# Kernel optimization log

Hardware: AMD Instinct MI355X
Metric: run time of the kernel (lower is better)

Reference implementation:

```python
import jax, jax.numpy as jnp
import numpy as np

HEADS = 16
DIM_HEAD = 64
QUERY_DIM = 1024


def setup_inputs() -> dict:
    key = jax.random.key(0)
    ks = jax.random.split(key, 5)
    B, S, D = 4, 2048, QUERY_DIM
    inner = HEADS * DIM_HEAD
    s = 0.02
    return {
        "x": jax.random.normal(ks[0], (B, S, D), dtype=jnp.float32),
        "Wq": jax.random.normal(ks[1], (D, inner), dtype=jnp.float32) * s,
        "Wk": jax.random.normal(ks[2], (D, inner), dtype=jnp.float32) * s,
        "Wv": jax.random.normal(ks[3], (D, inner), dtype=jnp.float32) * s,
        "Wo": jax.random.normal(ks[4], (inner, D), dtype=jnp.float32) * s,
    }


def reference(x, Wq, Wk, Wv, Wo):
    B, S, D = x.shape
    h, d = HEADS, DIM_HEAD
    scale = d ** (-0.5)
    # projections -> [B, h, S, d]
    q = (x @ Wq).reshape(B, S, h, d).transpose(0, 2, 1, 3)
    k = (x @ Wk).reshape(B, S, h, d).transpose(0, 2, 1, 3)
    v = (x @ Wv).reshape(B, S, h, d).transpose(0, 2, 1, 3)
    # scores [B, h, S, S]
    attn = jnp.einsum("bhqd,bhkd->bhqk", q, k) * scale
    attn = jax.nn.softmax(attn, axis=-1)
    out = jnp.einsum("bhqk,bhkd->bhqd", attn, v)
    out = out.transpose(0, 2, 1, 3).reshape(B, S, h * d)
    return out @ Wo
```

## Files before the change

### kernel.cpp

```cpp
#include <hip/hip_runtime.h>
#include <cstddef>

#define BATCH  4
#define SLEN   2048
#define NHEADS 16
#define DHEAD  64
#define DMODEL 1024

typedef __attribute__((ext_vector_type(8))) short short8;
typedef __attribute__((ext_vector_type(4))) float f32x4;

__device__ inline unsigned short f2bf(float f) {
    union { float f; unsigned int u; } v; v.f = f;
    unsigned int r = v.u + 0x7fffu + ((v.u >> 16) & 1u);
    return (unsigned short)(r >> 16);
}

__device__ inline float fast_exp2(float x) {
#if __has_builtin(__builtin_amdgcn_exp2f)
    return __builtin_amdgcn_exp2f(x);
#else
    return __expf(x * 0.69314718f);
#endif
}

__device__ inline void gload_lds16(const unsigned short* g, unsigned short* l) {
    __builtin_amdgcn_global_load_lds(
        (const __attribute__((address_space(1))) void*)g,
        (__attribute__((address_space(3))) void*)l, 16, 0, 0);
}

__global__ __launch_bounds__(256)
void convert_bf16(const float* __restrict__ src, unsigned short* __restrict__ dst, int n8)
{
    const int i = blockIdx.x * 256 + threadIdx.x;
    if (i >= n8) return;
    const float4 a = ((const float4*)src)[2 * i];
    const float4 b = ((const float4*)src)[2 * i + 1];
    short8 o;
    o[0] = (short)f2bf(a.x); o[1] = (short)f2bf(a.y);
    o[2] = (short)f2bf(a.z); o[3] = (short)f2bf(a.w);
    o[4] = (short)f2bf(b.x); o[5] = (short)f2bf(b.y);
    o[6] = (short)f2bf(b.z); o[7] = (short)f2bf(b.w);
    ((short8*)dst)[i] = o;
}

__global__ __launch_bounds__(256)
void wtrans(const float* __restrict__ W0, const float* __restrict__ W1,
            const float* __restrict__ W2, const float* __restrict__ W3,
            unsigned short* __restrict__ T0, unsigned short* __restrict__ T1,
            unsigned short* __restrict__ T2, unsigned short* __restrict__ T3)
{
    const int z = blockIdx.z;
    const float* W = (z == 0) ? W0 : (z == 1) ? W1 : (z == 2) ? W2 : W3;
    unsigned short* Wt = (z == 0) ? T0 : (z == 1) ? T1 : (z == 2) ? T2 : T3;

    __shared__ unsigned short T[64 * 72];
    const int tid = threadIdx.x;
    const int n0 = blockIdx.x * 64, k0 = blockIdx.y * 64;

    #pragma unroll
    for (int it = 0; it < 2; it++) {
        const int t2 = it * 256 + tid;
        const int row = t2 >> 3, col8 = (t2 & 7) * 8;
        const float4 a = *(const float4*)(W + (size_t)(k0 + row) * DMODEL + n0 + col8);
        const float4 b = *(const float4*)(W + (size_t)(k0 + row) * DMODEL + n0 + col8 + 4);
        short8 o;
        o[0] = (short)f2bf(a.x); o[1] = (short)f2bf(a.y);
        o[2] = (short)f2bf(a.z); o[3] = (short)f2bf(a.w);
        o[4] = (short)f2bf(b.x); o[5] = (short)f2bf(b.y);
        o[6] = (short)f2bf(b.z); o[7] = (short)f2bf(b.w);
        *(short8*)&T[row * 72 + col8] = o;
    }
    __syncthreads();
    #pragma unroll
    for (int it = 0; it < 2; it++) {
        const int t2 = it * 256 + tid;
        const int nn = t2 >> 3, k8 = (t2 & 7) * 8;
        short8 v;
        #pragma unroll
        for (int j = 0; j < 8; j++) v[j] = (short)T[(k8 + j) * 72 + nn];
        *(short8*)(Wt + (size_t)(n0 + nn) * DMODEL + k0 + k8) = v;
    }
}

__global__ __launch_bounds__(256)
void transpose_v(const unsigned short* __restrict__ vb, unsigned short* __restrict__ vtb)
{
    __shared__ unsigned short T[64 * 72];
    const int tid = threadIdx.x, st = blockIdx.x, bh = blockIdx.y;
    const int b = bh >> 4, h = bh & 15;
    const size_t bh_base = ((size_t)b * SLEN * NHEADS + h) * 64;

    #pragma unroll
    for (int it = 0; it < 2; it++) {
        const int t2 = it * 256 + tid;
        const int row = t2 >> 3, col8 = (t2 & 7) * 8;
        *(short8*)&T[row * 72 + col8] =
            *(const short8*)(vb + bh_base + (size_t)(st * 64 + row) * (NHEADS * 64) + col8);
    }
    __syncthreads();
    #pragma unroll
    for (int it = 0; it < 2; it++) {
        const int t2 = it * 256 + tid;
        const int dd = t2 >> 3, s8 = (t2 & 7) * 8;
        short8 v;
        #pragma unroll
        for (int j = 0; j < 8; j++) v[j] = (short)T[(s8 + j) * 72 + dd];
        *(short8*)(vtb + ((size_t)bh * 64 + dd) * SLEN + st * 64 + s8) = v;
    }
}

template<int OUTF32>
__global__ __launch_bounds__(256)
void gemm_bf16(const unsigned short* __restrict__ A,
               const unsigned short* __restrict__ B0,
               const unsigned short* __restrict__ B1,
               const unsigned short* __restrict__ B2,
               void* __restrict__ C0v, void* __restrict__ C1v, void* __restrict__ C2v)
{
    constexpr int N = DMODEL, K = DMODEL;
    __shared__ unsigned short As[128 * 64];
    __shared__ unsigned short Bs[128 * 64];

    const int z = blockIdx.z;
    const unsigned short* Bw = (z == 0) ? B0 : (z == 1) ? B1 : B2;
    void* Cv = (z == 0) ? C0v : (z == 1) ? C1v : C2v;

    const int tid  = threadIdx.x;
    const int lane = tid & 63;
    const int wave = tid >> 6;
    const int c  = lane & 15, qd = lane >> 4;
    const int wr = wave >> 1, wc = wave & 1;
    const int m0 = blockIdx.y * 128, n0 = blockIdx.x * 128;

    const unsigned short* ag[4];
    const unsigned short* bg[4];
    unsigned short* al[4];
    unsigned short* bl[4];
    #pragma unroll
    for (int j = 0; j < 4; j++) {
        const int cid = j * 256 + tid;
        const int row = cid >> 3;
        const int k8  = (cid & 7) ^ (row & 7);
        ag[j] = A  + (size_t)(m0 + row) * K + k8 * 8;
        bg[j] = Bw + (size_t)(n0 + row) * K + k8 * 8;
        al[j] = &As[cid * 8];
        bl[j] = &Bs[cid * 8];
    }

    f32x4 acc[4][4];
    #pragma unroll
    for (int mb = 0; mb < 4; mb++)
        #pragma unroll
        for (int nb = 0; nb < 4; nb++)
            #pragma unroll
            for (int r = 0; r < 4; r++) acc[mb][nb][r] = 0.f;

    for (int k0 = 0; k0 < K; k0 += 64) {
        __syncthreads();
        #pragma unroll
        for (int j = 0; j < 4; j++) {
            gload_lds16(ag[j], al[j]);
            gload_lds16(bg[j], bl[j]);
            ag[j] += 64; bg[j] += 64;
        }
        __syncthreads();

        #pragma unroll
        for (int ks = 0; ks < 2; ks++) {
            const int sw = (ks * 4 + qd) ^ (c & 7);
            short8 af[4], bf[4];
            #pragma unroll
            for (int mb = 0; mb < 4; mb++)
                af[mb] = *(const short8*)&As[((wr * 64 + mb * 16 + c) * 8 + sw) * 8];
            #pragma unroll
            for (int nb = 0; nb < 4; nb++)
                bf[nb] = *(const short8*)&Bs[((wc * 64 + nb * 16 + c) * 8 + sw) * 8];
            #pragma unroll
            for (int mb = 0; mb < 4; mb++)
                #pragma unroll
                for (int nb = 0; nb < 4; nb++)
                    acc[mb][nb] = __builtin_amdgcn_mfma_f32_16x16x32_bf16(
                        af[mb], bf[nb], acc[mb][nb], 0, 0, 0);
        }
    }

    const int mbase = m0 + wr * 64 + qd * 4;
    const int nbase = n0 + wc * 64 + c;
    if (OUTF32) {
        float* C = (float*)Cv;
        #pragma unroll
        for (int mb = 0; mb < 4; mb++)
            #pragma unroll
            for (int nb = 0; nb < 4; nb++)
                #pragma unroll
                for (int r = 0; r < 4; r++)
                    C[(size_t)(mbase + mb * 16 + r) * N + nbase + nb * 16] = acc[mb][nb][r];
    } else {
        unsigned short* C = (unsigned short*)Cv;
        #pragma unroll
        for (int mb = 0; mb < 4; mb++)
            #pragma unroll
            for (int nb = 0; nb < 4; nb++)
                #pragma unroll
                for (int r = 0; r < 4; r++)
                    C[(size_t)(mbase + mb * 16 + r) * N + nbase + nb * 16] = f2bf(acc[mb][nb][r]);
    }
}

__global__ __launch_bounds__(256)
void attn_mfma2(const unsigned short* __restrict__ qb,
                const unsigned short* __restrict__ kb,
                const unsigned short* __restrict__ vtb,
                unsigned short* __restrict__ O)
{
    __shared__ unsigned short lds[17408];
    unsigned short* Ks = lds;
    unsigned short* Vs = lds + 4096;

    const int tid = threadIdx.x;
    const int w   = tid >> 6, ln = tid & 63;
    const int c   = ln & 15, qd = ln >> 4;
    unsigned short* Pw = lds + 8192 + w * 2048;

    const int qt = blockIdx.x, bh = blockIdx.y;
    const int b = bh >> 4, h = bh & 15;
    const size_t bh_base = ((size_t)b * SLEN * NHEADS + h) * 64;
    constexpr int RS = NHEADS * 64;
    constexpr float SCL2 = 0.18033688f;

    const int srow = ln >> 3;
    const int sk8  = (ln & 7) ^ srow;
    const unsigned short* kg0 = kb + bh_base + (size_t)(w * 8 + srow) * RS + sk8 * 8;
    const unsigned short* kg1 = kg0 + (size_t)32 * RS;
    const unsigned short* vg0 = vtb + ((size_t)bh * 64 + w * 8 + srow) * SLEN + sk8 * 8;
    const unsigned short* vg1 = vg0 + (size_t)32 * SLEN;
    unsigned short* kl0 = &Ks[(w * 64 + ln) * 8];
    unsigned short* kl1 = kl0 + 2048;
    unsigned short* vl0 = &Vs[(w * 64 + ln) * 8];
    unsigned short* vl1 = vl0 + 2048;

    short8 qf[2][2];
    #pragma unroll
    for (int qh = 0; qh < 2; qh++)
        #pragma unroll
        for (int ks = 0; ks < 2; ks++)
            qf[qh][ks] = *(const short8*)(qb + bh_base +
                (size_t)(qt * 128 + w * 32 + qh * 16 + c) * RS + ks * 32 + qd * 8);

    f32x4 acc[4][2];
    #pragma unroll
    for (int mb = 0; mb < 4; mb++)
        #pragma unroll
        for (int qh = 0; qh < 2; qh++)
            #pragma unroll
            for (int r = 0; r < 4; r++) acc[mb][qh][r] = 0.f;
    float lsum[2] = {0.f, 0.f};
    const int X0 = (0 * 4 + qd) ^ (c & 7);
    const int X1 = (1 * 4 + qd) ^ (c & 7);

    for (int kt = 0; kt < SLEN / 64; kt++) {
        __syncthreads();
        gload_lds16(kg0, kl0); gload_lds16(kg1, kl1);
        gload_lds16(vg0, vl0); gload_lds16(vg1, vl1);
        kg0 += (size_t)64 * RS; kg1 += (size_t)64 * RS; vg0 += 64; vg1 += 64;
        __syncthreads();

        f32x4 sacc[4][2];
        #pragma unroll
        for (int kbI = 0; kbI < 4; kbI++)
            #pragma unroll
            for (int qh = 0; qh < 2; qh++)
                #pragma unroll
                for (int r = 0; r < 4; r++) sacc[kbI][qh][r] = 0.f;
        #pragma unroll
        for (int ks = 0; ks < 2; ks++) {
            const int X = ks ? X1 : X0;
            #pragma unroll
            for (int kbI = 0; kbI < 4; kbI++) {
                short8 kf = *(const short8*)&Ks[((kbI * 16 + c) * 8 + X) * 8];
                sacc[kbI][0] = __builtin_amdgcn_mfma_f32_16x16x32_bf16(kf, qf[0][ks], sacc[kbI][0], 0, 0, 0);
                sacc[kbI][1] = __builtin_amdgcn_mfma_f32_16x16x32_bf16(kf, qf[1][ks], sacc[kbI][1], 0, 0, 0);
            }
        }

        #pragma unroll
        for (int kbI = 0; kbI < 4; kbI++)
            #pragma unroll
            for (int qh = 0; qh < 2; qh++) {
                const float p0 = fast_exp2(sacc[kbI][qh][0] * SCL2);
                const float p1 = fast_exp2(sacc[kbI][qh][1] * SCL2);
                const float p2 = fast_exp2(sacc[kbI][qh][2] * SCL2);
                const float p3 = fast_exp2(sacc[kbI][qh][3] * SCL2);
                lsum[qh] += (p0 + p1) + (p2 + p3);
                uint2 pk;
                pk.x = __builtin_amdgcn_perm(__float_as_uint(p1), __float_as_uint(p0), 0x07060302u);
                pk.y = __builtin_amdgcn_perm(__float_as_uint(p3), __float_as_uint(p2), 0x07060302u);
                *(uint2*)&Pw[(qh * 16 + c) * 64 +
                             ((kbI * 2 + (qd >> 1)) ^ (c & 7)) * 8 + (qd & 1) * 4] = pk;
            }
        __builtin_amdgcn_wave_barrier();

        #pragma unroll
        for (int ks = 0; ks < 2; ks++) {
            const int X = ks ? X1 : X0;
            short8 pf0 = *(const short8*)&Pw[(0 * 16 + c) * 64 + X * 8];
            short8 pf1 = *(const short8*)&Pw[(1 * 16 + c) * 64 + X * 8];
            #pragma unroll
            for (int mb = 0; mb < 4; mb++) {
                short8 vf = *(const short8*)&Vs[((mb * 16 + c) * 8 + X) * 8];
                acc[mb][0] = __builtin_amdgcn_mfma_f32_16x16x32_bf16(vf, pf0, acc[mb][0], 0, 0, 0);
                acc[mb][1] = __builtin_amdgcn_mfma_f32_16x16x32_bf16(vf, pf1, acc[mb][1], 0, 0, 0);
            }
        }
    }

    __syncthreads();
    float inv[2];
    #pragma unroll
    for (int qh = 0; qh < 2; qh++) {
        float l = lsum[qh];
        l += __shfl_xor(l, 16);
        l += __shfl_xor(l, 32);
        inv[qh] = 1.001953125f / l;
    }
    float* Ot = (float*)lds;
    #pragma unroll
    for (int mb = 0; mb < 4; mb++)
        #pragma unroll
        for (int qh = 0; qh < 2; qh++)
            #pragma unroll
            for (int r = 0; r < 4; r++)
                Ot[(w * 32 + qh * 16 + c) * 68 + mb * 16 + qd * 4 + r] = acc[mb][qh][r] * inv[qh];
    __syncthreads();
    #pragma unroll
    for (int it = 0; it < 4; it++) {
        const int t2 = it * 256 + tid;
        const int row = t2 >> 3, col8 = (t2 & 7) * 8;
        short8 o;
        #pragma unroll
        for (int j = 0; j < 8; j++) o[j] = (short)f2bf(Ot[row * 68 + col8 + j]);
        *(short8*)(O + bh_base + (size_t)(qt * 128 + row) * RS + col8) = o;
    }
}

extern "C" void kernel_launch(void* const* d_in, const int* in_sizes, int n_in,
                              void* d_out, int out_size, void* d_ws, size_t ws_size,
                              hipStream_t stream)
{
    const float* x  = (const float*)d_in[0];
    const float* Wq = (const float*)d_in[1];
    const float* Wk = (const float*)d_in[2];
    const float* Wv = (const float*)d_in[3];
    const float* Wo = (const float*)d_in[4];
    float* out = (float*)d_out;

    const size_t per = (size_t)BATCH * SLEN * NHEADS * DHEAD;
    const size_t wsz = (size_t)DMODEL * DMODEL;
    unsigned short* qb  = (unsigned short*)d_ws;
    unsigned short* kb  = qb  + per;
    unsigned short* vb  = kb  + per;
    unsigned short* vtb = vb  + per;
    unsigned short* xb  = vtb + per;
    unsigned short* wtq = xb  + per;
    unsigned short* wtk = wtq + wsz;
    unsigned short* wtv = wtk + wsz;
    unsigned short* wto = wtv + wsz;

    dim3 blk(256);
    convert_bf16<<<dim3((int)(per / 2048)), blk, 0, stream>>>(x, xb, (int)(per / 8));
    wtrans<<<dim3(16, 16, 4), blk, 0, stream>>>(Wq, Wk, Wv, Wo, wtq, wtk, wtv, wto);

    gemm_bf16<0><<<dim3(8, 64, 3), blk, 0, stream>>>(xb, wtq, wtk, wtv, qb, kb, vb);

    transpose_v<<<dim3(32, 64), blk, 0, stream>>>(vb, vtb);
    attn_mfma2<<<dim3(SLEN / 128, BATCH * NHEADS), blk, 0, stream>>>(qb, kb, vtb, qb);

    gemm_bf16<1><<<dim3(8, 64, 1), blk, 0, stream>>>(qb, wto, wto, wto, out, out, out);
}
```

Before: 315.9 us.

## Fuse V transpose into QKV GEMM epilogue and double attention query tile

The QKV projection GEMM now writes V directly in transposed [b,h,d,s] layout from its epilogue, so the separate transpose_v kernel and its intermediate buffer go away. The attention kernel grows to 256 queries per block (64 per wave), which reuses each loaded K/V tile across twice as many queries and halves the number of K/V loads per query. Its epilogue converts to bf16 in per-wave LDS and stores without block-wide syncs. In exchange there is more register and LDS pressure, fewer blocks (512), and the V epilogue stores are narrower and strided.

```diff
diff --git a/kernel.cpp b/kernel.cpp
--- a/kernel.cpp
+++ b/kernel.cpp
@@ -84,34 +84,7 @@
     }
 }
 
-__global__ __launch_bounds__(256)
-void transpose_v(const unsigned short* __restrict__ vb, unsigned short* __restrict__ vtb)
-{
-    __shared__ unsigned short T[64 * 72];
-    const int tid = threadIdx.x, st = blockIdx.x, bh = blockIdx.y;
-    const int b = bh >> 4, h = bh & 15;
-    const size_t bh_base = ((size_t)b * SLEN * NHEADS + h) * 64;
-
-    #pragma unroll
-    for (int it = 0; it < 2; it++) {
-        const int t2 = it * 256 + tid;
-        const int row = t2 >> 3, col8 = (t2 & 7) * 8;
-        *(short8*)&T[row * 72 + col8] =
-            *(const short8*)(vb + bh_base + (size_t)(st * 64 + row) * (NHEADS * 64) + col8);
-    }
-    __syncthreads();
-    #pragma unroll
-    for (int it = 0; it < 2; it++) {
-        const int t2 = it * 256 + tid;
-        const int dd = t2 >> 3, s8 = (t2 & 7) * 8;
-        short8 v;
-        #pragma unroll
-        for (int j = 0; j < 8; j++) v[j] = (short)T[(s8 + j) * 72 + dd];
-        *(short8*)(vtb + ((size_t)bh * 64 + dd) * SLEN + st * 64 + s8) = v;
-    }
-}
-
-template<int OUTF32>
+template<int KIND>
 __global__ __launch_bounds__(256)
 void gemm_bf16(const unsigned short* __restrict__ A,
                const unsigned short* __restrict__ B0,
@@ -188,7 +161,7 @@
 
     const int mbase = m0 + wr * 64 + qd * 4;
     const int nbase = n0 + wc * 64 + c;
-    if (OUTF32) {
+    if (KIND == 1) {
         float* C = (float*)Cv;
         #pragma unroll
         for (int mb = 0; mb < 4; mb++)
@@ -197,32 +170,47 @@
                 #pragma unroll
                 for (int r = 0; r < 4; r++)
                     C[(size_t)(mbase + mb * 16 + r) * N + nbase + nb * 16] = acc[mb][nb][r];
+    } else if (z != 2) {
+        unsigned short* C = (unsigned short*)Cv;
+        #pragma unroll
+        for (int mb = 0; mb < 4; mb++)
+            #pragma unroll
+            for (int nb = 0; nb < 4; nb++)
+                #pragma unroll
+                for (int r = 0; r < 4; r++)
+                    C[(size_t)(mbase + mb * 16 + r) * N + nbase + nb * 16] = f2bf(acc[mb][nb][r]);
     } else {
         unsigned short* C = (unsigned short*)Cv;
-        #pragma unroll
-        for (int mb = 0; mb < 4; mb++)
-            #pragma unroll
-            for (int nb = 0; nb < 4; nb++)
-                #pragma unroll
-                for (int r = 0; r < 4; r++)
-                    C[(size_t)(mbase + mb * 16 + r) * N + nbase + nb * 16] = f2bf(acc[mb][nb][r]);
-    }
-}
-
-__global__ __launch_bounds__(256)
-void attn_mfma2(const unsigned short* __restrict__ qb,
+        const int b = mbase >> 11;
+        #pragma unroll
+        for (int mb = 0; mb < 4; mb++) {
+            const int s = (mbase + mb * 16) & 2047;
+            #pragma unroll
+            for (int nb = 0; nb < 4; nb++) {
+                const int n = nbase + nb * 16;
+                const int h = n >> 6, dd = n & 63;
+                ushort4 val = make_ushort4(f2bf(acc[mb][nb][0]), f2bf(acc[mb][nb][1]),
+                                           f2bf(acc[mb][nb][2]), f2bf(acc[mb][nb][3]));
+                *(ushort4*)(C + ((size_t)((b * 16 + h) * 64 + dd)) * SLEN + s) = val;
+            }
+        }
+    }
+}
+
+__global__ __launch_bounds__(256, 2)
+void attn_mfma3(const unsigned short* __restrict__ qb,
                 const unsigned short* __restrict__ kb,
                 const unsigned short* __restrict__ vtb,
                 unsigned short* __restrict__ O)
 {
-    __shared__ unsigned short lds[17408];
+    __shared__ unsigned short lds[26624];
     unsigned short* Ks = lds;
     unsigned short* Vs = lds + 4096;
 
     const int tid = threadIdx.x;
     const int w   = tid >> 6, ln = tid & 63;
     const int c   = ln & 15, qd = ln >> 4;
-    unsigned short* Pw = lds + 8192 + w * 2048;
+    unsigned short* Pw = lds + 8192 + w * 4608;
 
     const int qt = blockIdx.x, bh = blockIdx.y;
     const int b = bh >> 4, h = bh & 15;
@@ -241,24 +229,24 @@
     unsigned short* vl0 = &Vs[(w * 64 + ln) * 8];
     unsigned short* vl1 = vl0 + 2048;
 
-    short8 qf[2][2];
-    #pragma unroll
-    for (int qh = 0; qh < 2; qh++)
+    short8 qf[4][2];
+    #pragma unroll
+    for (int qh = 0; qh < 4; qh++)
         #pragma unroll
         for (int ks = 0; ks < 2; ks++)
             qf[qh][ks] = *(const short8*)(qb + bh_base +
-                (size_t)(qt * 128 + w * 32 + qh * 16 + c) * RS + ks * 32 + qd * 8);
-
-    f32x4 acc[4][2];
+                (size_t)(qt * 256 + w * 64 + qh * 16 + c) * RS + ks * 32 + qd * 8);
+
+    f32x4 acc[4][4];
     #pragma unroll
     for (int mb = 0; mb < 4; mb++)
         #pragma unroll
-        for (int qh = 0; qh < 2; qh++)
+        for (int qh = 0; qh < 4; qh++)
             #pragma unroll
             for (int r = 0; r < 4; r++) acc[mb][qh][r] = 0.f;
-    float lsum[2] = {0.f, 0.f};
-    const int X0 = (0 * 4 + qd) ^ (c & 7);
-    const int X1 = (1 * 4 + qd) ^ (c & 7);
+    float lsum[4] = {0.f, 0.f, 0.f, 0.f};
+    const int X0 = qd ^ (c & 7);
+    const int X1 = (4 + qd) ^ (c & 7);
 
     for (int kt = 0; kt < SLEN / 64; kt++) {
         __syncthreads();
@@ -267,81 +255,80 @@
         kg0 += (size_t)64 * RS; kg1 += (size_t)64 * RS; vg0 += 64; vg1 += 64;
         __syncthreads();
 
-        f32x4 sacc[4][2];
-        #pragma unroll
-        for (int kbI = 0; kbI < 4; kbI++)
-            #pragma unroll
-            for (int qh = 0; qh < 2; qh++)
-                #pragma unroll
-                for (int r = 0; r < 4; r++) sacc[kbI][qh][r] = 0.f;
-        #pragma unroll
-        for (int ks = 0; ks < 2; ks++) {
-            const int X = ks ? X1 : X0;
-            #pragma unroll
-            for (int kbI = 0; kbI < 4; kbI++) {
+        #pragma unroll
+        for (int kbI = 0; kbI < 4; kbI++) {
+            f32x4 sacc[4];
+            #pragma unroll
+            for (int qh = 0; qh < 4; qh++)
+                #pragma unroll
+                for (int r = 0; r < 4; r++) sacc[qh][r] = 0.f;
+            #pragma unroll
+            for (int ks = 0; ks < 2; ks++) {
+                const int X = ks ? X1 : X0;
                 short8 kf = *(const short8*)&Ks[((kbI * 16 + c) * 8 + X) * 8];
-                sacc[kbI][0] = __builtin_amdgcn_mfma_f32_16x16x32_bf16(kf, qf[0][ks], sacc[kbI][0], 0, 0, 0);
-                sacc[kbI][1] = __builtin_amdgcn_mfma_f32_16x16x32_bf16(kf, qf[1][ks], sacc[kbI][1], 0, 0, 0);
+                #pragma unroll
+                for (int qh = 0; qh < 4; qh++)
+                    sacc[qh] = __builtin_amdgcn_mfma_f32_16x16x32_bf16(
+                        kf, qf[qh][ks], sacc[qh], 0, 0, 0);
             }
-        }
-
-        #pragma unroll
-        for (int kbI = 0; kbI < 4; kbI++)
-            #pragma unroll
-            for (int qh = 0; qh < 2; qh++) {
-                const float p0 = fast_exp2(sacc[kbI][qh][0] * SCL2);
-                const float p1 = fast_exp2(sacc[kbI][qh][1] * SCL2);
-                const float p2 = fast_exp2(sacc[kbI][qh][2] * SCL2);
-                const float p3 = fast_exp2(sacc[kbI][qh][3] * SCL2);
+            const int pchunk = ((kbI * 2 + (qd >> 1)) ^ (c & 7)) * 8 + (qd & 1) * 4;
+            #pragma unroll
+            for (int qh = 0; qh < 4; qh++) {
+                const float p0 = fast_exp2(sacc[qh][0] * SCL2);
+                const float p1 = fast_exp2(sacc[qh][1] * SCL2);
+                const float p2 = fast_exp2(sacc[qh][2] * SCL2);
+                const float p3 = fast_exp2(sacc[qh][3] * SCL2);
                 lsum[qh] += (p0 + p1) + (p2 + p3);
                 uint2 pk;
                 pk.x = __builtin_amdgcn_perm(__float_as_uint(p1), __float_as_uint(p0), 0x07060302u);
                 pk.y = __builtin_amdgcn_perm(__float_as_uint(p3), __float_as_uint(p2), 0x07060302u);
-                *(uint2*)&Pw[(qh * 16 + c) * 64 +
-                             ((kbI * 2 + (qd >> 1)) ^ (c & 7)) * 8 + (qd & 1) * 4] = pk;
+                *(uint2*)&Pw[(qh * 16 + c) * 64 + pchunk] = pk;
             }
+        }
         __builtin_amdgcn_wave_barrier();
 
         #pragma unroll
         for (int ks = 0; ks < 2; ks++) {
             const int X = ks ? X1 : X0;
-            short8 pf0 = *(const short8*)&Pw[(0 * 16 + c) * 64 + X * 8];
-            short8 pf1 = *(const short8*)&Pw[(1 * 16 + c) * 64 + X * 8];
+            short8 pf[4];
+            #pragma unroll
+            for (int qh = 0; qh < 4; qh++)
+                pf[qh] = *(const short8*)&Pw[(qh * 16 + c) * 64 + X * 8];
             #pragma unroll
             for (int mb = 0; mb < 4; mb++) {
                 short8 vf = *(const short8*)&Vs[((mb * 16 + c) * 8 + X) * 8];
-                acc[mb][0] = __builtin_amdgcn_mfma_f32_16x16x32_bf16(vf, pf0, acc[mb][0], 0, 0, 0);
-                acc[mb][1] = __builtin_amdgcn_mfma_f32_16x16x32_bf16(vf, pf1, acc[mb][1], 0, 0, 0);
+                #pragma unroll
+                for (int qh = 0; qh < 4; qh++)
+                    acc[mb][qh] = __builtin_amdgcn_mfma_f32_16x16x32_bf16(
+                        vf, pf[qh], acc[mb][qh], 0, 0, 0);
             }
         }
     }
 
-    __syncthreads();
-    float inv[2];
-    #pragma unroll
-    for (int qh = 0; qh < 2; qh++) {
+    float inv[4];
+    #pragma unroll
+    for (int qh = 0; qh < 4; qh++) {
         float l = lsum[qh];
         l += __shfl_xor(l, 16);
         l += __shfl_xor(l, 32);
         inv[qh] = 1.001953125f / l;
     }
-    float* Ot = (float*)lds;
+    __builtin_amdgcn_wave_barrier();
     #pragma unroll
     for (int mb = 0; mb < 4; mb++)
         #pragma unroll
-        for (int qh = 0; qh < 2; qh++)
+        for (int qh = 0; qh < 4; qh++)
             #pragma unroll
             for (int r = 0; r < 4; r++)
-                Ot[(w * 32 + qh * 16 + c) * 68 + mb * 16 + qd * 4 + r] = acc[mb][qh][r] * inv[qh];
-    __syncthreads();
-    #pragma unroll
-    for (int it = 0; it < 4; it++) {
-        const int t2 = it * 256 + tid;
+                Pw[(qh * 16 + c) * 72 + mb * 16 + qd * 4 + r] =
+                    f2bf(acc[mb][qh][r] * inv[qh]);
+    __builtin_amdgcn_wave_barrier();
+    #pragma unroll
+    for (int it = 0; it < 8; it++) {
+        const int t2 = it * 64 + ln;
         const int row = t2 >> 3, col8 = (t2 & 7) * 8;
-        short8 o;
-        #pragma unroll
-        for (int j = 0; j < 8; j++) o[j] = (short)f2bf(Ot[row * 68 + col8 + j]);
-        *(short8*)(O + bh_base + (size_t)(qt * 128 + row) * RS + col8) = o;
+        short8 o = *(const short8*)&Pw[row * 72 + col8];
+        *(short8*)(O + bh_base + (size_t)(qt * 256 + w * 64 + row) * RS + col8) = o;
     }
 }
 
@@ -360,8 +347,7 @@
     const size_t wsz = (size_t)DMODEL * DMODEL;
     unsigned short* qb  = (unsigned short*)d_ws;
     unsigned short* kb  = qb  + per;
-    unsigned short* vb  = kb  + per;
-    unsigned short* vtb = vb  + per;
+    unsigned short* vtb = kb  + per;
     unsigned short* xb  = vtb + per;
     unsigned short* wtq = xb  + per;
     unsigned short* wtk = wtq + wsz;
@@ -372,10 +358,9 @@
     convert_bf16<<<dim3((int)(per / 2048)), blk, 0, stream>>>(x, xb, (int)(per / 8));
     wtrans<<<dim3(16, 16, 4), blk, 0, stream>>>(Wq, Wk, Wv, Wo, wtq, wtk, wtv, wto);
 
-    gemm_bf16<0><<<dim3(8, 64, 3), blk, 0, stream>>>(xb, wtq, wtk, wtv, qb, kb, vb);
-
-    transpose_v<<<dim3(32, 64), blk, 0, stream>>>(vb, vtb);
-    attn_mfma2<<<dim3(SLEN / 128, BATCH * NHEADS), blk, 0, stream>>>(qb, kb, vtb, qb);
+    gemm_bf16<0><<<dim3(8, 64, 3), blk, 0, stream>>>(xb, wtq, wtk, wtv, qb, kb, vtb);
+
+    attn_mfma3<<<dim3(SLEN / 256, BATCH * NHEADS), blk, 0, stream>>>(qb, kb, vtb, qb);
 
     gemm_bf16<1><<<dim3(8, 64, 1), blk, 0, stream>>>(qb, wto, wto, wto, out, out, out);
 }
```

Result: faster. 280.7 us (-11.1%).
